# Optimization experiments

Hardware: AMD Instinct MI355X
Metric: run time of the kernel (lower is better)

## Reference

```python
import jax, jax.numpy as jnp
import numpy as np

B, T, D, H = 128, 1024, 128, 128

def setup_inputs() -> dict:
    key = jax.random.key(0)
    ks = jax.random.split(key, 7)
    scale = 0.05
    return {
        "x": jax.random.normal(ks[0], (B, T, D), dtype=jnp.float32),
        "h0": jnp.zeros((B, H), dtype=jnp.float32),
        "U": jax.random.normal(ks[1], (D, H), dtype=jnp.float32) * scale,
        "W": jax.random.normal(ks[2], (H, H), dtype=jnp.float32) * scale,
        "V": jax.random.normal(ks[3], (H, H), dtype=jnp.float32) * scale,
        "bu": jnp.zeros((H,), dtype=jnp.float32),
        "bw": jnp.zeros((H,), dtype=jnp.float32),
        "bv": jnp.zeros((H,), dtype=jnp.float32),
    }

def reference(x, h0, U, W, V, bu, bw, bv):
    # Precompute input projection for all timesteps in one big GEMM: [B,T,H]
    xu = jnp.einsum('btd,dh->bth', x, U) + bu

    def step(h, xu_t):
        # st = tanh(x@U + bu + h@W + bw)
        st = jnp.tanh(xu_t + h @ W + bw)
        # o = tanh(st@V + bv)
        o = jnp.tanh(st @ V + bv)
        return st, o

    # scan over time: xu transposed to [T,B,H]
    _, o_seq = jax.lax.scan(step, h0, jnp.swapaxes(xu, 0, 1))
    return jnp.swapaxes(o_seq, 0, 1)  # [B,T,H]
```

## Files before the change

kernel.cpp:

```cpp
#include <hip/hip_runtime.h>

#define B_ 128
#define T_ 1024
#define D_ 128
#define H_ 128

typedef short bf16x8 __attribute__((ext_vector_type(8)));
typedef float f32x4 __attribute__((ext_vector_type(4)));

__device__ inline short f2bf(float f) {
    union { float f; unsigned u; } v; v.f = f;
    unsigned u = v.u;
    unsigned r = (u + 0x7fffu + ((u >> 16) & 1u)) >> 16;
    return (short)r;
}

__device__ inline float fast_tanh(float x) {
    float e = __expf(2.0f * x);
    return 1.0f - __fdividef(2.0f, 1.0f + e);
}

__device__ inline void lds_barrier() {
    asm volatile("s_waitcnt lgkmcnt(0)\n\ts_barrier" ::: "memory");
}

__global__ __launch_bounds__(256) void xu_kernel(
    const float* __restrict__ x, const float* __restrict__ U,
    const float* __restrict__ bu, float* __restrict__ out)
{
    __shared__ bf16x8 uf[2048];
    const int tid  = threadIdx.x;
    const int lane = tid & 63;
    const int wave = tid >> 6;
    const int q = lane >> 4, c = lane & 15;

    for (int s = tid; s < 2048; s += 256) {
        int l = s & 63, kk = (s >> 6) & 3, nt = s >> 8;
        int lq = l >> 4, lc = l & 15;
        int kbase = 32 * kk + 8 * lq;
        int col = 16 * nt + lc;
        bf16x8 f;
#pragma unroll
        for (int j = 0; j < 8; ++j)
            f[j] = f2bf(U[(kbase + j) * H_ + col]);
        uf[s] = f;
    }

    float bub[8];
#pragma unroll
    for (int nt = 0; nt < 8; ++nt) bub[nt] = bu[16 * nt + c];

    __syncthreads();

    for (int it = 0; it < 4; ++it) {
        const int row0 = (blockIdx.x * 4 + it) * 64 + wave * 16;

        bf16x8 af[4];
#pragma unroll
        for (int kk = 0; kk < 4; ++kk) {
            const float* px = x + (row0 + (lane & 15)) * D_ + 32 * kk + 8 * q;
            f32x4 a0 = *(const f32x4*)px;
            f32x4 a1 = *(const f32x4*)(px + 4);
            bf16x8 f;
            f[0] = f2bf(a0[0]); f[1] = f2bf(a0[1]); f[2] = f2bf(a0[2]); f[3] = f2bf(a0[3]);
            f[4] = f2bf(a1[0]); f[5] = f2bf(a1[1]); f[6] = f2bf(a1[2]); f[7] = f2bf(a1[3]);
            af[kk] = f;
        }

#pragma unroll
        for (int nt = 0; nt < 8; ++nt) {
            f32x4 acc = {bub[nt], bub[nt], bub[nt], bub[nt]};
#pragma unroll
            for (int kk = 0; kk < 4; ++kk)
                acc = __builtin_amdgcn_mfma_f32_16x16x32_bf16(af[kk], uf[(nt * 4 + kk) * 64 + lane], acc, 0, 0, 0);
            float* po = out + (row0 + 4 * q) * H_ + 16 * nt + c;
#pragma unroll
            for (int r = 0; r < 4; ++r)
                po[r * H_] = acc[r];
        }
    }
}

__global__ __launch_bounds__(1024) void scan_kernel(
    float* __restrict__ out,
    const float* __restrict__ h0,
    const float* __restrict__ W, const float* __restrict__ V,
    const float* __restrict__ bw, const float* __restrict__ bv)
{
    __shared__ __align__(16) short st[2][16][136];

    const int tid  = threadIdx.x;
    const int lane = tid & 63;
    const int wave = tid >> 6;
    const bool is_h = wave < 8;
    const int n  = wave & 7;
    const int q = lane >> 4, c = lane & 15;
    const int c0 = 16 * n;
    const int b0 = blockIdx.x * 16;

    const float* M = is_h ? W : V;
    bf16x8 wf[4];
#pragma unroll
    for (int kk = 0; kk < 4; ++kk) {
        int kbase = 32 * kk + 8 * q;
        bf16x8 f;
#pragma unroll
        for (int j = 0; j < 8; ++j)
            f[j] = f2bf(M[(kbase + j) * H_ + c0 + c]);
        wf[kk] = f;
    }
    const float vbias = is_h ? bw[c0 + c] : bv[c0 + c];

    {
        int m = wave;
        int k0 = lane * 2;
        const float* ph = h0 + (b0 + m) * H_ + k0;
        float2 hv = *(const float2*)ph;
        union { short s2[2]; unsigned u; } pk;
        pk.s2[0] = f2bf(hv.x);
        pk.s2[1] = f2bf(hv.y);
        *(unsigned*)&st[1][m][k0] = pk.u;
    }

    const int obase = (b0 + 4 * q) * T_ * H_ + c0 + c;

    f32x4 xubuf[8];
    if (is_h) {
#pragma unroll
        for (int u = 0; u < 8; ++u)
#pragma unroll
            for (int r = 0; r < 4; ++r)
                xubuf[u][r] = out[obase + r * T_ * H_ + u * H_];
    }
    lds_barrier();

    for (int tb = 0; tb < T_ / 8; ++tb) {
#pragma unroll
        for (int u = 0; u < 8; ++u) {
            const int t = tb * 8 + u;
            const int pr = (u + 1) & 1;
            const int pw = u & 1;

            if (is_h) {
                f32x4 xu_c = xubuf[u];
                if (t + 8 < T_) {
#pragma unroll
                    for (int r = 0; r < 4; ++r)
                        xubuf[u][r] = out[obase + r * T_ * H_ + (t + 8) * H_];
                }
                bf16x8 af[4];
#pragma unroll
                for (int kk = 0; kk < 4; ++kk)
                    af[kk] = *(const bf16x8*)&st[pr][lane & 15][32 * kk + 8 * q];
                f32x4 accA, accB;
#pragma unroll
                for (int r = 0; r < 4; ++r) { accA[r] = xu_c[r] + vbias; accB[r] = 0.f; }
                accA = __builtin_amdgcn_mfma_f32_16x16x32_bf16(af[0], wf[0], accA, 0, 0, 0);
                accB = __builtin_amdgcn_mfma_f32_16x16x32_bf16(af[1], wf[1], accB, 0, 0, 0);
                accA = __builtin_amdgcn_mfma_f32_16x16x32_bf16(af[2], wf[2], accA, 0, 0, 0);
                accB = __builtin_amdgcn_mfma_f32_16x16x32_bf16(af[3], wf[3], accB, 0, 0, 0);
#pragma unroll
                for (int r = 0; r < 4; ++r) {
                    float s = fast_tanh(accA[r] + accB[r]);
                    st[pw][4 * q + r][c0 + c] = f2bf(s);
                }
            } else if (t > 0) {
                bf16x8 af[4];
#pragma unroll
                for (int kk = 0; kk < 4; ++kk)
                    af[kk] = *(const bf16x8*)&st[pr][lane & 15][32 * kk + 8 * q];
                f32x4 acc = {vbias, vbias, vbias, vbias};
#pragma unroll
                for (int kk = 0; kk < 4; ++kk)
                    acc = __builtin_amdgcn_mfma_f32_16x16x32_bf16(af[kk], wf[kk], acc, 0, 0, 0);
#pragma unroll
                for (int r = 0; r < 4; ++r)
                    out[obase + r * T_ * H_ + (t - 1) * H_] = fast_tanh(acc[r]);
            }
            lds_barrier();
        }
    }

    if (!is_h) {
        bf16x8 af[4];
#pragma unroll
        for (int kk = 0; kk < 4; ++kk)
            af[kk] = *(const bf16x8*)&st[1][lane & 15][32 * kk + 8 * q];
        f32x4 acc = {vbias, vbias, vbias, vbias};
#pragma unroll
        for (int kk = 0; kk < 4; ++kk)
            acc = __builtin_amdgcn_mfma_f32_16x16x32_bf16(af[kk], wf[kk], acc, 0, 0, 0);
#pragma unroll
        for (int r = 0; r < 4; ++r)
            out[obase + r * T_ * H_ + (T_ - 1) * H_] = fast_tanh(acc[r]);
    }
}

extern "C" void kernel_launch(void* const* d_in, const int* in_sizes, int n_in,
                              void* d_out, int out_size, void* d_ws, size_t ws_size,
                              hipStream_t stream) {
    const float* x  = (const float*)d_in[0];
    const float* h0 = (const float*)d_in[1];
    const float* U  = (const float*)d_in[2];
    const float* W  = (const float*)d_in[3];
    const float* V  = (const float*)d_in[4];
    const float* bu = (const float*)d_in[5];
    const float* bw = (const float*)d_in[6];
    const float* bv = (const float*)d_in[7];
    float* out = (float*)d_out;

    xu_kernel<<<512, 256, 0, stream>>>(x, U, bu, out);
    scan_kernel<<<8, 1024, 0, stream>>>(out, h0, W, V, bw, bv);
}
```

Measured before the change: 896.0 us.

## Split output projection out of serial scan into separate parallel kernel

The o = tanh(st@V+bv) projection moves out of the sequential scan kernel into a third, fully parallel kernel that reads bf16 hidden states written to workspace. The scan block shrinks to 8 waves that only do the recurrence, and it reads xu from a layout the xu kernel writes in per-step contiguous order with bw folded into the bias. This is meant to shorten the serial critical path per timestep and make its global loads coalesced. In exchange it adds an extra kernel launch and a round trip of hidden states through global memory.

```diff
diff --git a/kernel.cpp b/kernel.cpp
--- a/kernel.cpp
+++ b/kernel.cpp
@@ -26,173 +26,213 @@
 
 __global__ __launch_bounds__(256) void xu_kernel(
     const float* __restrict__ x, const float* __restrict__ U,
-    const float* __restrict__ bu, float* __restrict__ out)
+    const float* __restrict__ bu, const float* __restrict__ bw,
+    float* __restrict__ xu_out)
 {
-    __shared__ bf16x8 uf[2048];
+    __shared__ short uf[16384];
     const int tid  = threadIdx.x;
     const int lane = tid & 63;
     const int wave = tid >> 6;
     const int q = lane >> 4, c = lane & 15;
 
-    for (int s = tid; s < 2048; s += 256) {
-        int l = s & 63, kk = (s >> 6) & 3, nt = s >> 8;
-        int lq = l >> 4, lc = l & 15;
-        int kbase = 32 * kk + 8 * lq;
-        int col = 16 * nt + lc;
-        bf16x8 f;
-#pragma unroll
-        for (int j = 0; j < 8; ++j)
-            f[j] = f2bf(U[(kbase + j) * H_ + col]);
-        uf[s] = f;
-    }
-
-    float bub[8];
-#pragma unroll
-    for (int nt = 0; nt < 8; ++nt) bub[nt] = bu[16 * nt + c];
-
-    __syncthreads();
-
-    for (int it = 0; it < 4; ++it) {
-        const int row0 = (blockIdx.x * 4 + it) * 64 + wave * 16;
-
-        bf16x8 af[4];
+    const int bg = blockIdx.x & 31;
+    const int tg = blockIdx.x >> 5;
+    const int b_base = bg * 4;
+    const int t0w = tg * 16 + wave * 4;
+
+#pragma unroll
+    for (int i = 0; i < 16; ++i) {
+        int f4 = i * 256 + tid;
+        int k   = f4 >> 5;
+        int hb  = (f4 & 31) * 4;
+        f32x4 v = *(const f32x4*)(U + k * H_ + hb);
+        int kk = k >> 5, lq = (k >> 3) & 3, j = k & 7;
+#pragma unroll
+        for (int e = 0; e < 4; ++e) {
+            int h = hb + e;
+            uf[(((h >> 4) * 4 + kk) * 64 + lq * 16 + (h & 15)) * 8 + j] = f2bf(v[e]);
+        }
+    }
+
+    float bias[8];
+#pragma unroll
+    for (int nt = 0; nt < 8; ++nt) bias[nt] = bu[16 * nt + c] + bw[16 * nt + c];
+
+    bf16x8 af[4];
+    {
+        const float* px = x + ((size_t)(b_base + (c & 3)) * T_ + (t0w + (c >> 2))) * D_ + 8 * q;
 #pragma unroll
         for (int kk = 0; kk < 4; ++kk) {
-            const float* px = x + (row0 + (lane & 15)) * D_ + 32 * kk + 8 * q;
-            f32x4 a0 = *(const f32x4*)px;
-            f32x4 a1 = *(const f32x4*)(px + 4);
+            f32x4 a0 = *(const f32x4*)(px + 32 * kk);
+            f32x4 a1 = *(const f32x4*)(px + 32 * kk + 4);
             bf16x8 f;
             f[0] = f2bf(a0[0]); f[1] = f2bf(a0[1]); f[2] = f2bf(a0[2]); f[3] = f2bf(a0[3]);
             f[4] = f2bf(a1[0]); f[5] = f2bf(a1[1]); f[6] = f2bf(a1[2]); f[7] = f2bf(a1[3]);
             af[kk] = f;
         }
-
-#pragma unroll
-        for (int nt = 0; nt < 8; ++nt) {
-            f32x4 acc = {bub[nt], bub[nt], bub[nt], bub[nt]};
-#pragma unroll
-            for (int kk = 0; kk < 4; ++kk)
-                acc = __builtin_amdgcn_mfma_f32_16x16x32_bf16(af[kk], uf[(nt * 4 + kk) * 64 + lane], acc, 0, 0, 0);
-            float* po = out + (row0 + 4 * q) * H_ + 16 * nt + c;
-#pragma unroll
-            for (int r = 0; r < 4; ++r)
-                po[r * H_] = acc[r];
-        }
-    }
-}
-
-__global__ __launch_bounds__(1024) void scan_kernel(
-    float* __restrict__ out,
+    }
+    __syncthreads();
+
+    const int blkb = bg >> 2;
+    const int qs   = bg & 3;
+    const int tC   = t0w + q;
+    float* pout = xu_out + (size_t)(tC * 8 + blkb) * 8 * 256 + (qs * 16 + c) * 4;
+
+#pragma unroll
+    for (int nt = 0; nt < 8; ++nt) {
+        f32x4 acc = {bias[nt], bias[nt], bias[nt], bias[nt]};
+#pragma unroll
+        for (int kk = 0; kk < 4; ++kk)
+            acc = __builtin_amdgcn_mfma_f32_16x16x32_bf16(
+                af[kk], *(const bf16x8*)&uf[((nt * 4 + kk) * 64 + lane) * 8], acc, 0, 0, 0);
+        *(f32x4*)(pout + nt * 256) = acc;
+    }
+}
+
+__global__ __launch_bounds__(512) void scan_kernel(
+    const float* __restrict__ xu,
+    short* __restrict__ st_ws,
     const float* __restrict__ h0,
-    const float* __restrict__ W, const float* __restrict__ V,
-    const float* __restrict__ bw, const float* __restrict__ bv)
+    const float* __restrict__ W)
 {
     __shared__ __align__(16) short st[2][16][136];
 
+    const int tid  = threadIdx.x;
+    const int lane = tid & 63;
+    const int n    = tid >> 6;
+    const int q = lane >> 4, c = lane & 15;
+    const int c0 = 16 * n;
+    const int blk = blockIdx.x;
+    const int b0  = blk * 16;
+
+    bf16x8 wf[4];
+#pragma unroll
+    for (int kk = 0; kk < 4; ++kk) {
+        bf16x8 f;
+#pragma unroll
+        for (int j = 0; j < 8; ++j)
+            f[j] = f2bf(W[(32 * kk + 8 * q + j) * H_ + c0 + c]);
+        wf[kk] = f;
+    }
+
+    {
+        int m  = tid >> 5;
+        int k0 = (tid & 31) * 4;
+        f32x4 hv = *(const f32x4*)(h0 + (b0 + m) * H_ + k0);
+        union { short s[4]; unsigned long long u; } pk;
+        pk.s[0] = f2bf(hv[0]); pk.s[1] = f2bf(hv[1]);
+        pk.s[2] = f2bf(hv[2]); pk.s[3] = f2bf(hv[3]);
+        *(unsigned long long*)&st[1][m][k0] = pk.u;
+    }
+
+    const float* pxu = xu + (blk * 8 + n) * 256 + lane * 4;
+    short* pst = st_ws + blk * 2048 + c * 128 + 8 * q;
+
+    f32x4 xubuf[4];
+#pragma unroll
+    for (int u = 0; u < 4; ++u)
+        xubuf[u] = *(const f32x4*)(pxu + u * 16384);
+
+    lds_barrier();
+
+    for (int tb = 0; tb < T_ / 4; ++tb) {
+#pragma unroll
+        for (int u = 0; u < 4; ++u) {
+            const int t  = tb * 4 + u;
+            const int pr = (u + 1) & 1;
+            const int pw = u & 1;
+
+            f32x4 accA = xubuf[u];
+            if (t + 4 < T_)
+                xubuf[u] = *(const f32x4*)(pxu + (t + 4) * 16384);
+
+            bf16x8 af[4];
+#pragma unroll
+            for (int kk = 0; kk < 4; ++kk)
+                af[kk] = *(const bf16x8*)&st[pr][c][32 * kk + 8 * q];
+
+            if (u > 0 || tb > 0) {
+                short* pp = pst + (t - 1) * 16384;
+#pragma unroll
+                for (int kk = 0; kk < 4; ++kk)
+                    *(bf16x8*)(pp + 32 * kk) = af[kk];
+            }
+
+            f32x4 accB = {0.f, 0.f, 0.f, 0.f};
+            accA = __builtin_amdgcn_mfma_f32_16x16x32_bf16(af[0], wf[0], accA, 0, 0, 0);
+            accB = __builtin_amdgcn_mfma_f32_16x16x32_bf16(af[1], wf[1], accB, 0, 0, 0);
+            accA = __builtin_amdgcn_mfma_f32_16x16x32_bf16(af[2], wf[2], accA, 0, 0, 0);
+            accB = __builtin_amdgcn_mfma_f32_16x16x32_bf16(af[3], wf[3], accB, 0, 0, 0);
+#pragma unroll
+            for (int r = 0; r < 4; ++r) {
+                float s = fast_tanh(accA[r] + accB[r]);
+                st[pw][4 * q + r][c0 + c] = f2bf(s);
+            }
+            lds_barrier();
+        }
+    }
+
+    {
+        short* pp = pst + (T_ - 1) * 16384;
+#pragma unroll
+        for (int kk = 0; kk < 4; ++kk) {
+            bf16x8 a = *(const bf16x8*)&st[1][c][32 * kk + 8 * q];
+            *(bf16x8*)(pp + 32 * kk) = a;
+        }
+    }
+}
+
+__global__ __launch_bounds__(256) void o_kernel(
+    const short* __restrict__ st_ws, const float* __restrict__ V,
+    const float* __restrict__ bv, float* __restrict__ out)
+{
+    __shared__ short vf[16384];
     const int tid  = threadIdx.x;
     const int lane = tid & 63;
     const int wave = tid >> 6;
-    const bool is_h = wave < 8;
-    const int n  = wave & 7;
     const int q = lane >> 4, c = lane & 15;
-    const int c0 = 16 * n;
-    const int b0 = blockIdx.x * 16;
-
-    const float* M = is_h ? W : V;
-    bf16x8 wf[4];
-#pragma unroll
-    for (int kk = 0; kk < 4; ++kk) {
-        int kbase = 32 * kk + 8 * q;
-        bf16x8 f;
-#pragma unroll
-        for (int j = 0; j < 8; ++j)
-            f[j] = f2bf(M[(kbase + j) * H_ + c0 + c]);
-        wf[kk] = f;
-    }
-    const float vbias = is_h ? bw[c0 + c] : bv[c0 + c];
-
-    {
-        int m = wave;
-        int k0 = lane * 2;
-        const float* ph = h0 + (b0 + m) * H_ + k0;
-        float2 hv = *(const float2*)ph;
-        union { short s2[2]; unsigned u; } pk;
-        pk.s2[0] = f2bf(hv.x);
-        pk.s2[1] = f2bf(hv.y);
-        *(unsigned*)&st[1][m][k0] = pk.u;
-    }
-
-    const int obase = (b0 + 4 * q) * T_ * H_ + c0 + c;
-
-    f32x4 xubuf[8];
-    if (is_h) {
-#pragma unroll
-        for (int u = 0; u < 8; ++u)
-#pragma unroll
-            for (int r = 0; r < 4; ++r)
-                xubuf[u][r] = out[obase + r * T_ * H_ + u * H_];
-    }
-    lds_barrier();
-
-    for (int tb = 0; tb < T_ / 8; ++tb) {
-#pragma unroll
-        for (int u = 0; u < 8; ++u) {
-            const int t = tb * 8 + u;
-            const int pr = (u + 1) & 1;
-            const int pw = u & 1;
-
-            if (is_h) {
-                f32x4 xu_c = xubuf[u];
-                if (t + 8 < T_) {
-#pragma unroll
-                    for (int r = 0; r < 4; ++r)
-                        xubuf[u][r] = out[obase + r * T_ * H_ + (t + 8) * H_];
-                }
-                bf16x8 af[4];
-#pragma unroll
-                for (int kk = 0; kk < 4; ++kk)
-                    af[kk] = *(const bf16x8*)&st[pr][lane & 15][32 * kk + 8 * q];
-                f32x4 accA, accB;
-#pragma unroll
-                for (int r = 0; r < 4; ++r) { accA[r] = xu_c[r] + vbias; accB[r] = 0.f; }
-                accA = __builtin_amdgcn_mfma_f32_16x16x32_bf16(af[0], wf[0], accA, 0, 0, 0);
-                accB = __builtin_amdgcn_mfma_f32_16x16x32_bf16(af[1], wf[1], accB, 0, 0, 0);
-                accA = __builtin_amdgcn_mfma_f32_16x16x32_bf16(af[2], wf[2], accA, 0, 0, 0);
-                accB = __builtin_amdgcn_mfma_f32_16x16x32_bf16(af[3], wf[3], accB, 0, 0, 0);
-#pragma unroll
-                for (int r = 0; r < 4; ++r) {
-                    float s = fast_tanh(accA[r] + accB[r]);
-                    st[pw][4 * q + r][c0 + c] = f2bf(s);
-                }
-            } else if (t > 0) {
-                bf16x8 af[4];
-#pragma unroll
-                for (int kk = 0; kk < 4; ++kk)
-                    af[kk] = *(const bf16x8*)&st[pr][lane & 15][32 * kk + 8 * q];
-                f32x4 acc = {vbias, vbias, vbias, vbias};
-#pragma unroll
-                for (int kk = 0; kk < 4; ++kk)
-                    acc = __builtin_amdgcn_mfma_f32_16x16x32_bf16(af[kk], wf[kk], acc, 0, 0, 0);
-#pragma unroll
-                for (int r = 0; r < 4; ++r)
-                    out[obase + r * T_ * H_ + (t - 1) * H_] = fast_tanh(acc[r]);
-            }
-            lds_barrier();
-        }
-    }
-
-    if (!is_h) {
-        bf16x8 af[4];
+
+#pragma unroll
+    for (int i = 0; i < 16; ++i) {
+        int f4 = i * 256 + tid;
+        int k  = f4 >> 5;
+        int hb = (f4 & 31) * 4;
+        f32x4 v = *(const f32x4*)(V + k * H_ + hb);
+        int kk = k >> 5, lq = (k >> 3) & 3, j = k & 7;
+#pragma unroll
+        for (int e = 0; e < 4; ++e) {
+            int h = hb + e;
+            vf[(((h >> 4) * 4 + kk) * 64 + lq * 16 + (h & 15)) * 8 + j] = f2bf(v[e]);
+        }
+    }
+
+    float bias[8];
+#pragma unroll
+    for (int nt = 0; nt < 8; ++nt) bias[nt] = bv[16 * nt + c];
+
+    const int p   = blockIdx.x * 4 + wave;
+    const int t   = p >> 3;
+    const int blk = p & 7;
+
+    const short* ps = st_ws + (size_t)p * 2048 + c * 128 + 8 * q;
+    bf16x8 af[4];
+#pragma unroll
+    for (int kk = 0; kk < 4; ++kk)
+        af[kk] = *(const bf16x8*)(ps + 32 * kk);
+
+    __syncthreads();
+
+    float* po = out + ((size_t)(blk * 16 + 4 * q) * T_ + t) * H_ + c;
+#pragma unroll
+    for (int nt = 0; nt < 8; ++nt) {
+        f32x4 acc = {bias[nt], bias[nt], bias[nt], bias[nt]};
 #pragma unroll
         for (int kk = 0; kk < 4; ++kk)
-            af[kk] = *(const bf16x8*)&st[1][lane & 15][32 * kk + 8 * q];
-        f32x4 acc = {vbias, vbias, vbias, vbias};
-#pragma unroll
-        for (int kk = 0; kk < 4; ++kk)
-            acc = __builtin_amdgcn_mfma_f32_16x16x32_bf16(af[kk], wf[kk], acc, 0, 0, 0);
+            acc = __builtin_amdgcn_mfma_f32_16x16x32_bf16(
+                af[kk], *(const bf16x8*)&vf[((nt * 4 + kk) * 64 + lane) * 8], acc, 0, 0, 0);
 #pragma unroll
         for (int r = 0; r < 4; ++r)
-            out[obase + r * T_ * H_ + (T_ - 1) * H_] = fast_tanh(acc[r]);
+            po[(size_t)r * T_ * H_ + 16 * nt] = fast_tanh(acc[r]);
     }
 }
 
@@ -208,7 +248,9 @@
     const float* bw = (const float*)d_in[6];
     const float* bv = (const float*)d_in[7];
     float* out = (float*)d_out;
-
-    xu_kernel<<<512, 256, 0, stream>>>(x, U, bu, out);
-    scan_kernel<<<8, 1024, 0, stream>>>(out, h0, W, V, bw, bv);
-}
+    short* st_ws = (short*)d_ws;
+
+    xu_kernel<<<2048, 256, 0, stream>>>(x, U, bu, bw, out);
+    scan_kernel<<<8, 512, 0, stream>>>(out, st_ws, h0, W);
+    o_kernel<<<2048, 256, 0, stream>>>(st_ws, V, bv, out);
+}
```

Result: slower. 1.177 ms (+31.4%).
